# Kernel optimization log

Hardware: AMD Instinct MI355X
Metric: run time of the kernel (lower is better)

The kernel has to match this reference:

```python
import jax, jax.numpy as jnp
import numpy as np

B, H, W, C = 16, 96, 96, 128
FOCAL_LEVEL = 3
FOCAL_WINDOW = 3
FOCAL_FACTOR = 2
LN_EPS = 1e-3  # keras LayerNormalization default epsilon


def dwconv_same(x, k):
    # x: [B,H,W,C], k: [kh,kw,1,C] depthwise kernel (feature_group_count=C)
    return jax.lax.conv_general_dilated(
        x, k, window_strides=(1, 1), padding='SAME',
        dimension_numbers=('NHWC', 'HWIO', 'NHWC'),
        feature_group_count=x.shape[-1])


def setup_inputs() -> dict:
    key = jax.random.key(0)
    ks = jax.random.split(key, 12)
    s = 0.02
    out_f = 2 * C + (FOCAL_LEVEL + 1)
    inp = {
        'x': jax.random.normal(ks[0], (B, H, W, C), dtype=jnp.float32),
        'Wf': jax.random.normal(ks[1], (C, out_f), dtype=jnp.float32) * s,
        'bf': jnp.zeros((out_f,), dtype=jnp.float32),
        'Wh': jax.random.normal(ks[2], (C, C), dtype=jnp.float32) * s,
        'bh': jnp.zeros((C,), dtype=jnp.float32),
        'gamma': jnp.ones((C,), dtype=jnp.float32),
        'beta': jnp.zeros((C,), dtype=jnp.float32),
        'Wp': jax.random.normal(ks[3], (C, C), dtype=jnp.float32) * s,
        'bp': jnp.zeros((C,), dtype=jnp.float32),
    }
    for l in range(FOCAL_LEVEL):
        kk = FOCAL_FACTOR * l + FOCAL_WINDOW  # 3, 5, 7
        inp[f'k{l}'] = jax.random.normal(ks[4 + l], (kk, kk, 1, C), dtype=jnp.float32) * s
    return inp


def reference(x, Wf, bf, k0, k1, k2, Wh, bh, gamma, beta, Wp, bp):
    gelu = lambda t: jax.nn.gelu(t, approximate=False)  # keras gelu is exact
    y = jnp.einsum('bhwc,cd->bhwd', x, Wf) + bf  # f(): [B,H,W,2C+L+1]
    q = y[..., :C]
    ctx = y[..., C:2 * C]
    gates = y[..., 2 * C:]  # [B,H,W,L+1]

    ctx_all = jnp.zeros_like(ctx)
    for l, k in enumerate((k0, k1, k2)):
        ctx = gelu(dwconv_same(ctx, k))
        ctx_all = ctx_all + ctx * gates[..., l:l + 1]

    ctx_global = gelu(jnp.mean(ctx, axis=(1, 2), keepdims=True))  # [B,1,1,C]
    ctx_all = ctx_all + ctx_global * gates[..., FOCAL_LEVEL:]

    modulator = jnp.einsum('bhwc,cd->bhwd', ctx_all, Wh) + bh  # 1x1 conv h()
    x_out = q * modulator

    # post-LN over channel dim
    mu = jnp.mean(x_out, axis=-1, keepdims=True)
    var = jnp.mean(jnp.square(x_out - mu), axis=-1, keepdims=True)
    x_out = (x_out - mu) * jax.lax.rsqrt(var + LN_EPS) * gamma + beta

    x_out = jnp.einsum('bhwc,cd->bhwd', x_out, Wp) + bp  # proj (dropout p=0)
    return x_out
```

## Files before the change

### kernel.cpp

```cpp
#include <hip/hip_runtime.h>
#include <math.h>

#define B_ 16
#define H_ 96
#define W_ 96
#define C_ 128
#define HW_ (H_*W_)
#define NTOK (B_*HW_)
#define NOUT 260

#define TH 16
#define TW 32
#define B0H 28
#define B0W 44
#define B1H 26
#define B1W 42
#define B2H 22
#define B2W 38

typedef unsigned short ushort_t;
typedef unsigned int uint_t;
typedef float f32x4 __attribute__((ext_vector_type(4)));
typedef float f32x2 __attribute__((ext_vector_type(2)));
typedef short bfrag __attribute__((ext_vector_type(8)));
typedef unsigned short us8 __attribute__((ext_vector_type(8)));

__device__ __forceinline__ float gelu_f(float t) {
    return 0.5f * t * (1.0f + erff(t * 0.7071067811865475f));
}
__device__ __forceinline__ float b2f(ushort_t u) {
    union { unsigned int i; float f; } t; t.i = (unsigned int)u << 16; return t.f;
}
__device__ __forceinline__ ushort_t f2b(float f) {
    union { float f; unsigned int i; } t; t.f = f;
    unsigned int lsb = (t.i >> 16) & 1u;
    t.i += 0x7fffu + lsb;
    return (ushort_t)(t.i >> 16);
}
__device__ __forceinline__ uint_t pk2(float a, float b) {
    uint_t r;
    asm("v_cvt_pk_bf16_f32 %0, %1, %2" : "=v"(r) : "v"(a), "v"(b));
    return r;
}
__device__ __forceinline__ void unp2(uint_t u, float& a, float& b) {
    union { unsigned int i; float f; } x, y;
    x.i = u << 16; y.i = u & 0xffff0000u;
    a = x.f; b = y.f;
}
__device__ __forceinline__ void unp8(const uint4 v, float* f) {
    unp2(v.x, f[0], f[1]); unp2(v.y, f[2], f[3]);
    unp2(v.z, f[4], f[5]); unp2(v.w, f[6], f[7]);
}
__device__ __forceinline__ uint4 pk8(const float* f) {
    uint4 v;
    v.x = pk2(f[0], f[1]); v.y = pk2(f[2], f[3]);
    v.z = pk2(f[4], f[5]); v.w = pk2(f[6], f[7]);
    return v;
}
__device__ __forceinline__ f32x2 unp2p(uint_t u) {
    union { uint_t i; float f; } a, b;
    a.i = u << 16; b.i = u & 0xffff0000u;
    f32x2 r; r.x = a.f; r.y = b.f; return r;
}
__device__ __forceinline__ void unp8p(const uint4 v, f32x2* d) {
    d[0] = unp2p(v.x); d[1] = unp2p(v.y); d[2] = unp2p(v.z); d[3] = unp2p(v.w);
}

__device__ __forceinline__ void split8_to(const float* f,
                                          ushort_t* __restrict__ hdst,
                                          ushort_t* __restrict__ ldst) {
    uint_t hp[4], lp[4];
    #pragma unroll
    for (int j = 0; j < 4; ++j) {
        const float a = f[2*j], b = f[2*j+1];
        const uint_t h = pk2(a, b);
        union { uint_t i; float f; } ha, hb;
        ha.i = h << 16; hb.i = h & 0xffff0000u;
        hp[j] = h;
        lp[j] = pk2(a - ha.f, b - hb.f);
    }
    *(uint4*)hdst = make_uint4(hp[0], hp[1], hp[2], hp[3]);
    *(uint4*)ldst = make_uint4(lp[0], lp[1], lp[2], lp[3]);
}

__global__ __launch_bounds__(128) void pack_weights(
    const float* __restrict__ Wf, const float* __restrict__ Wh,
    const float* __restrict__ Wp, ushort_t* __restrict__ pk)
{
    const int n = blockIdx.x, mat = blockIdx.y, k = threadIdx.x;
    if (mat == 4 && n >= 16) return;
    float v;
    if (mat == 0)      v = Wf[(size_t)k * NOUT + n];
    else if (mat == 1) v = Wf[(size_t)k * NOUT + C_ + n];
    else if (mat == 2) v = Wh[(size_t)k * C_ + n];
    else if (mat == 3) v = Wp[(size_t)k * C_ + n];
    else               v = (n < 4) ? Wf[(size_t)k * NOUT + 2*C_ + n] : 0.0f;
    const ushort_t h = f2b(v);
    const ushort_t l = f2b(v - b2f(h));
    ushort_t* base = pk + (size_t)mat * (2 * C_ * C_);
    const int lo_off = (mat == 4) ? 16 * C_ : C_ * C_;
    base[n * C_ + k] = h;
    base[lo_off + n * C_ + k] = l;
}

template <bool A_LO>
__device__ __forceinline__ void mfma_gemm64(
    const ushort_t (*Ah)[136], const ushort_t (*Al)[136],
    const ushort_t* __restrict__ Bh, const ushort_t* __restrict__ Bl,
    int lane, int n0, f32x4 acc[4][2])
{
    const int ar = lane & 15;
    const int ak = (lane >> 4) << 3;
    #pragma unroll
    for (int kk = 0; kk < 4; ++kk) {
        const int kb = (kk << 5) + ak;
        const bfrag bh0 = *(const bfrag*)(Bh + (((n0      + ar) << 7) + kb));
        const bfrag bh1 = *(const bfrag*)(Bh + (((n0 + 16 + ar) << 7) + kb));
        const bfrag bl0 = *(const bfrag*)(Bl + (((n0      + ar) << 7) + kb));
        const bfrag bl1 = *(const bfrag*)(Bl + (((n0 + 16 + ar) << 7) + kb));
        #pragma unroll
        for (int m = 0; m < 4; ++m) {
            const bfrag ah = *(const bfrag*)&Ah[(m << 4) + ar][kb];
            if constexpr (A_LO) {
                const bfrag al = *(const bfrag*)&Al[(m << 4) + ar][kb];
                acc[m][0] = __builtin_amdgcn_mfma_f32_16x16x32_bf16(al, bh0, acc[m][0], 0, 0, 0);
                acc[m][1] = __builtin_amdgcn_mfma_f32_16x16x32_bf16(al, bh1, acc[m][1], 0, 0, 0);
            }
            acc[m][0] = __builtin_amdgcn_mfma_f32_16x16x32_bf16(ah, bl0, acc[m][0], 0, 0, 0);
            acc[m][1] = __builtin_amdgcn_mfma_f32_16x16x32_bf16(ah, bl1, acc[m][1], 0, 0, 0);
            acc[m][0] = __builtin_amdgcn_mfma_f32_16x16x32_bf16(ah, bh0, acc[m][0], 0, 0, 0);
            acc[m][1] = __builtin_amdgcn_mfma_f32_16x16x32_bf16(ah, bh1, acc[m][1], 0, 0, 0);
        }
    }
}

__device__ __forceinline__ void stage_split_f32(
    const float* __restrict__ src, int tid,
    ushort_t (*Ah)[136], ushort_t (*Al)[136])
{
    #pragma unroll
    for (int p = 0; p < 4; ++p) {
        const int i  = tid + (p << 8);
        const int t  = i >> 4;
        const int c8 = (i & 15) << 3;
        const float4 v0 = *(const float4*)(src + (size_t)t * C_ + c8);
        const float4 v1 = *(const float4*)(src + (size_t)t * C_ + c8 + 4);
        const float f[8] = {v0.x, v0.y, v0.z, v0.w, v1.x, v1.y, v1.z, v1.w};
        split8_to(f, &Ah[t][c8], &Al[t][c8]);
    }
}

__global__ __launch_bounds__(256) void gemm_ctx_gates_mfma(
    const float* __restrict__ x, const float* __restrict__ bf,
    const ushort_t* __restrict__ pk,
    ushort_t* __restrict__ ctx, float* __restrict__ gates,
    float* __restrict__ csum)
{
    __shared__ ushort_t Abuf[2][64][136];
    const int tid  = threadIdx.x;
    const int tok0 = blockIdx.x * 64;
    const int lane = tid & 63;
    const int n0   = (tid >> 6) << 5;

    if (blockIdx.x < 8) csum[blockIdx.x * 256 + tid] = 0.0f;

    stage_split_f32(x + (size_t)tok0 * C_, tid, Abuf[0], Abuf[1]);
    __syncthreads();

    f32x4 acc[4][2] = {};
    {
        const ushort_t* Bh = pk + (size_t)1 * (2 * C_ * C_);
        const ushort_t* Bl = Bh + C_ * C_;
        mfma_gemm64<true>(Abuf[0], Abuf[1], Bh, Bl, lane, n0, acc);
    }

    {
        const int w  = tid >> 6;
        const int ar = lane & 15;
        const int ak = (lane >> 4) << 3;
        const ushort_t* Gh = pk + (size_t)4 * (2 * C_ * C_);
        const ushort_t* Gl = Gh + 16 * C_;
        f32x4 gacc = {};
        #pragma unroll
        for (int kk = 0; kk < 4; ++kk) {
            const int kb = (kk << 5) + ak;
            const bfrag gh = *(const bfrag*)(Gh + ((ar << 7) + kb));
            const bfrag gl = *(const bfrag*)(Gl + ((ar << 7) + kb));
            const bfrag ah = *(const bfrag*)&Abuf[0][(w << 4) + ar][kb];
            const bfrag al = *(const bfrag*)&Abuf[1][(w << 4) + ar][kb];
            gacc = __builtin_amdgcn_mfma_f32_16x16x32_bf16(al, gh, gacc, 0, 0, 0);
            gacc = __builtin_amdgcn_mfma_f32_16x16x32_bf16(ah, gl, gacc, 0, 0, 0);
            gacc = __builtin_amdgcn_mfma_f32_16x16x32_bf16(ah, gh, gacc, 0, 0, 0);
        }
        if (ar < 4) {
            const int rg = (lane >> 4) << 2;
            #pragma unroll
            for (int r = 0; r < 4; ++r)
                gates[(size_t)(tok0 + (w << 4) + rg + r) * 4 + ar] = gacc[r] + bf[2*C_ + ar];
        }
    }
    __syncthreads();

    {
        const int ar = lane & 15;
        const int rg = (lane >> 4) << 2;
        #pragma unroll
        for (int n = 0; n < 2; ++n) {
            const int col = n0 + (n << 4) + ar;
            const float bias = bf[C_ + col];
            #pragma unroll
            for (int m = 0; m < 4; ++m) {
                const int rowb = (m << 4) + rg;
                const uint_t p0 = pk2(acc[m][n][0] + bias, acc[m][n][1] + bias);
                const uint_t p1 = pk2(acc[m][n][2] + bias, acc[m][n][3] + bias);
                Abuf[0][rowb + 0][col] = (ushort_t)p0;
                Abuf[0][rowb + 1][col] = (ushort_t)(p0 >> 16);
                Abuf[0][rowb + 2][col] = (ushort_t)p1;
                Abuf[0][rowb + 3][col] = (ushort_t)(p1 >> 16);
            }
        }
    }
    __syncthreads();

    #pragma unroll
    for (int p = 0; p < 4; ++p) {
        const int i  = tid + (p << 8);
        const int cg = i >> 6;
        const int t  = i & 63;
        *(uint4*)(ctx + (((size_t)cg * NTOK + tok0 + t) << 3))
            = *(const uint4*)&Abuf[0][t][cg << 3];
    }
}

__global__ __launch_bounds__(256, 4) void focal_conv_fused(
    const ushort_t* __restrict__ ctx_in,
    const float* __restrict__ k0w, const float* __restrict__ k1w,
    const float* __restrict__ k2w,
    const float* __restrict__ gates,
    ushort_t* __restrict__ ctx_all,
    float* __restrict__ csum)
{
    __shared__ uint4 bufA[B0H*B0W];
    __shared__ uint4 buf1[B1H*B1W];
    __shared__ float wts[(9+25+49)*8];

    const int tid  = threadIdx.x;
    const int cg   = blockIdx.x;
    const int tile = blockIdx.y;
    const int bb   = blockIdx.z;
    const int wt   = tile % 3, ht = tile / 3;
    const int c0   = cg << 3;
    const int h0   = ht * TH, w0 = wt * TW;

    if (tid < 166) {
        const int f = tid << 2;
        const float* src; int r;
        if (f < 72)       { r = f;       src = k0w; }
        else if (f < 272) { r = f - 72;  src = k1w; }
        else              { r = f - 272; src = k2w; }
        const int tap = r >> 3, off = r & 7;
        *(float4*)&wts[f] = *(const float4*)(src + tap * C_ + c0 + off);
    }

    const ushort_t* cin = ctx_in + (((size_t)cg * NTOK + (size_t)bb * HW_) << 3);
    for (int i = tid; i < B0H*B0W; i += 256) {
        const int r = i / B0W, q = i - r * B0W;
        const int hh = h0 - 6 + r, ww = w0 - 6 + q;
        uint4 v = make_uint4(0u, 0u, 0u, 0u);
        if ((unsigned)hh < (unsigned)H_ && (unsigned)ww < (unsigned)W_)
            v = *(const uint4*)(cin + ((size_t)(hh * W_ + ww) << 3));
        bufA[i] = v;
    }
    __syncthreads();

    {
        int iv[5], ecp[5], boff[5];
        #pragma unroll
        for (int p = 0; p < 5; ++p) {
            const int e = tid + (p << 8);
            iv[p] = (e < B1H*B1W);
            const int ec = iv[p] ? e : 0;
            ecp[p] = ec;
            boff[p] = (ec / B1W) * B0W + (ec % B1W);
        }
        f32x2 acc[5][4] = {};
        #pragma unroll 1
        for (int a = 0; a < 3; ++a) {
            #pragma unroll
            for (int b = 0; b < 3; ++b) {
                f32x2 wv[4];
                #pragma unroll
                for (int c = 0; c < 4; ++c)
                    wv[c] = *(const f32x2*)&wts[(a*3+b)*8 + 2*c];
                const int off = a * B0W + b;
                #pragma unroll
                for (int p = 0; p < 5; ++p) {
                    f32x2 d[4]; unp8p(bufA[boff[p] + off], d);
                    #pragma unroll
                    for (int c = 0; c < 4; ++c)
                        acc[p][c] = __builtin_elementwise_fma(d[c], wv[c], acc[p][c]);
                }
            }
        }
        __syncthreads();
        #pragma unroll
        for (int p = 0; p < 5; ++p) if (iv[p]) {
            float g[8];
            #pragma unroll
            for (int c = 0; c < 4; ++c) {
                g[2*c]   = gelu_f(acc[p][c].x);
                g[2*c+1] = gelu_f(acc[p][c].y);
            }
            buf1[ecp[p]] = pk8(g);
        }
    }
    __syncthreads();

    {
        int iv[4], ecp[4], boff[4];
        #pragma unroll
        for (int p = 0; p < 4; ++p) {
            const int e = tid + (p << 8);
            iv[p] = (e < B2H*B2W);
            const int ec = iv[p] ? e : 0;
            ecp[p] = ec;
            boff[p] = (ec / B2W) * B1W + (ec % B2W);
        }
        f32x2 acc[4][4] = {};
        #pragma unroll 1
        for (int a = 0; a < 5; ++a) {
            #pragma unroll
            for (int b = 0; b < 5; ++b) {
                f32x2 wv[4];
                #pragma unroll
                for (int c = 0; c < 4; ++c)
                    wv[c] = *(const f32x2*)&wts[72 + (a*5+b)*8 + 2*c];
                const int off = a * B1W + b;
                #pragma unroll
                for (int p = 0; p < 4; ++p) {
                    f32x2 d[4]; unp8p(buf1[boff[p] + off], d);
                    #pragma unroll
                    for (int c = 0; c < 4; ++c)
                        acc[p][c] = __builtin_elementwise_fma(d[c], wv[c], acc[p][c]);
                }
            }
        }
        __syncthreads();
        #pragma unroll
        for (int p = 0; p < 4; ++p) if (iv[p]) {
            float g[8];
            #pragma unroll
            for (int c = 0; c < 4; ++c) {
                g[2*c]   = gelu_f(acc[p][c].x);
                g[2*c+1] = gelu_f(acc[p][c].y);
            }
            bufA[ecp[p]] = pk8(g);
        }
    }
    __syncthreads();

    float lsum[8] = {};
    {
        const int th0 = tid >> 5, tw0 = tid & 31;
        f32x2 acc[2][4] = {};
        #pragma unroll 1
        for (int a = 0; a < 7; ++a) {
            #pragma unroll
            for (int b = 0; b < 7; ++b) {
                f32x2 wv[4];
                #pragma unroll
                for (int c = 0; c < 4; ++c)
                    wv[c] = *(const f32x2*)&wts[272 + (a*7+b)*8 + 2*c];
                #pragma unroll
                for (int p = 0; p < 2; ++p) {
                    const int th = th0 + (p << 3);
                    f32x2 d[4]; unp8p(bufA[(th + a)*B2W + (tw0 + b)], d);
                    #pragma unroll
                    for (int c = 0; c < 4; ++c)
                        acc[p][c] = __builtin_elementwise_fma(d[c], wv[c], acc[p][c]);
                }
            }
        }
        #pragma unroll
        for (int p = 0; p < 2; ++p) {
            const int th = th0 + (p << 3);
            float ctx3[8];
            #pragma unroll
            for (int c = 0; c < 4; ++c) {
                ctx3[2*c]   = gelu_f(acc[p][c].x);
                ctx3[2*c+1] = gelu_f(acc[p][c].y);
            }
            #pragma unroll
            for (int c = 0; c < 8; ++c) lsum[c] += ctx3[c];
            float d1[8]; unp8(buf1[(5+th)*B1W + (5+tw0)], d1);
            float d2[8]; unp8(bufA[(th+3)*B2W + (tw0+3)], d2);
            const size_t pix = (size_t)bb * HW_ + (size_t)(h0 + th) * W_ + (w0 + tw0);
            const float4 gt = *(const float4*)(gates + pix * 4);
            float o[8];
            #pragma unroll
            for (int c = 0; c < 8; ++c)
                o[c] = d1[c] * gt.x + d2[c] * gt.y + ctx3[c] * gt.z;
            *(uint4*)(ctx_all + pix * C_ + c0) = pk8(o);
        }
    }

    __syncthreads();
    float* red = (float*)bufA;
    #pragma unroll
    for (int c = 0; c < 8; ++c) red[c*256 + tid] = lsum[c];
    __syncthreads();
    for (int off = 128; off > 0; off >>= 1) {
        if (tid < off) {
            #pragma unroll
            for (int c = 0; c < 8; ++c)
                red[c*256 + tid] += red[c*256 + tid + off];
        }
        __syncthreads();
    }
    if (tid < 8) atomicAdd(&csum[bb * C_ + c0 + tid], red[tid * 256]);
}

__global__ __launch_bounds__(128) void glob_mod(
    const float* __restrict__ csum, const float* __restrict__ Wh,
    float* __restrict__ whc)
{
    __shared__ float cg[128];
    const int b = blockIdx.x, n = threadIdx.x;
    cg[n] = gelu_f(csum[b * C_ + n] * (1.0f / (float)HW_));
    __syncthreads();
    float s = 0.f;
    #pragma unroll 8
    for (int k = 0; k < C_; ++k)
        s = fmaf(cg[k], Wh[(size_t)k * C_ + n], s);
    whc[b * C_ + n] = s;
}

__global__ __launch_bounds__(256) void modq_ln_out_mfma(
    const ushort_t* __restrict__ ctx_all, const float* __restrict__ whc,
    const float* __restrict__ gates, const float* __restrict__ x,
    const ushort_t* __restrict__ pk, const float* __restrict__ bf,
    const float* __restrict__ bh, const float* __restrict__ gamma,
    const float* __restrict__ beta, const float* __restrict__ bp,
    float* __restrict__ out)
{
    __shared__ ushort_t Abuf[2][64][136];
    __shared__ float g3s[64];
    __shared__ float whcs[128];
    __shared__ float mu_s[64];
    __shared__ float rs_s[64];
    __shared__ f32x2 part[64][4];
    float (*xs)[132] = (float(*)[132])&Abuf[0][0][0];
    ushort_t (*xlnb)[136] = (ushort_t(*)[136])&Abuf[0][0][0];

    const int tid  = threadIdx.x;
    const int tok0 = blockIdx.x * 64;
    const int bidx = tok0 / HW_;
    const int lane = tid & 63;
    const int n0   = (tid >> 6) << 5;
    const int ar   = lane & 15;
    const int rg   = (lane >> 4) << 2;

    #pragma unroll
    for (int p = 0; p < 4; ++p) {
        const int i  = tid + (p << 8);
        const int t  = i >> 4;
        const int c8 = (i & 15) << 3;
        *(us8*)&Abuf[0][t][c8] = *(const us8*)(ctx_all + (size_t)(tok0 + t) * C_ + c8);
    }
    if (tid < 64)           g3s[tid]        = gates[(size_t)(tok0 + tid) * 4 + 3];
    else if (tid < 192)     whcs[tid - 64]  = whc[bidx * C_ + (tid - 64)];
    __syncthreads();

    f32x4 am[4][2] = {};
    {
        const ushort_t* Bh2 = pk + (size_t)2 * (2 * C_ * C_);
        const ushort_t* Bl2 = Bh2 + C_ * C_;
        mfma_gemm64<false>(Abuf[0], Abuf[0], Bh2, Bl2, lane, n0, am);
    }
    __syncthreads();

    stage_split_f32(x + (size_t)tok0 * C_, tid, Abuf[0], Abuf[1]);
    __syncthreads();

    f32x4 aq[4][2] = {};
    {
        const ushort_t* Bh0 = pk;
        const ushort_t* Bl0 = Bh0 + C_ * C_;
        mfma_gemm64<true>(Abuf[0], Abuf[1], Bh0, Bl0, lane, n0, aq);
    }
    __syncthreads();

    {
        #pragma unroll
        for (int n = 0; n < 2; ++n) {
            const int col = n0 + (n << 4) + ar;
            const float bfv = bf[col];
            const float bhv = bh[col];
            const float whv = whcs[col];
            #pragma unroll
            for (int m = 0; m < 4; ++m)
                #pragma unroll
                for (int r = 0; r < 4; ++r) {
                    const int row = (m << 4) + rg + r;
                    const float mod = am[m][n][r] + g3s[row] * whv + bhv;
                    xs[row][col] = (aq[m][n][r] + bfv) * mod;
                }
        }
    }
    __syncthreads();

    {
        const int tt = tid >> 2;
        const int qq = tid & 3;
        float s = 0.f, s2 = 0.f;
        #pragma unroll
        for (int c = 0; c < 32; c += 4) {
            const float4 v = *(const float4*)&xs[tt][(qq << 5) + c];
            s  += v.x + v.y + v.z + v.w;
            s2 += v.x*v.x + v.y*v.y + v.z*v.z + v.w*v.w;
        }
        f32x2 pr; pr.x = s; pr.y = s2;
        part[tt][qq] = pr;
    }
    __syncthreads();
    if (tid < 64) {
        const f32x2 p0 = part[tid][0], p1 = part[tid][1];
        const f32x2 p2 = part[tid][2], p3 = part[tid][3];
        const float s  = (p0.x + p1.x) + (p2.x + p3.x);
        const float s2 = (p0.y + p1.y) + (p2.y + p3.y);
        const float mu  = s * (1.0f / 128.0f);
        const float var = s2 * (1.0f / 128.0f) - mu * mu;
        mu_s[tid] = mu;
        rs_s[tid] = rsqrtf(var + 0.001f);
    }
    __syncthreads();

    {
        const int tt = tid >> 2;
        const int c0b = (tid & 3) << 5;
        const float mu = mu_s[tt], rs = rs_s[tt];
        uint_t xw[16];
        #pragma unroll
        for (int j = 0; j < 8; ++j) {
            const int c = c0b + (j << 2);
            const float4 v  = *(const float4*)&xs[tt][c];
            const float4 gm = *(const float4*)(gamma + c);
            const float4 bt = *(const float4*)(beta + c);
            xw[2*j]   = pk2((v.x - mu) * rs * gm.x + bt.x,
                            (v.y - mu) * rs * gm.y + bt.y);
            xw[2*j+1] = pk2((v.z - mu) * rs * gm.z + bt.z,
                            (v.w - mu) * rs * gm.w + bt.w);
        }
        __syncthreads();
        #pragma unroll
        for (int j = 0; j < 4; ++j)
            *(uint4*)&xlnb[tt][c0b + (j << 3)] = *(uint4*)&xw[4*j];
    }
    __syncthreads();

    f32x4 ao[4][2] = {};
    {
        const ushort_t* Bh3 = pk + (size_t)3 * (2 * C_ * C_);
        const ushort_t* Bl3 = Bh3 + C_ * C_;
        mfma_gemm64<false>((const ushort_t(*)[136])xlnb,
                           (const ushort_t(*)[136])xlnb, Bh3, Bl3, lane, n0, ao);
    }
    {
        #pragma unroll
        for (int n = 0; n < 2; ++n) {
            const int col = n0 + (n << 4) + ar;
            const float bpv = bp[col];
            #pragma unroll
            for (int m = 0; m < 4; ++m)
                #pragma unroll
                for (int r = 0; r < 4; ++r) {
                    const int row = (m << 4) + rg + r;
                    out[(size_t)(tok0 + row) * C_ + col] = ao[m][n][r] + bpv;
                }
        }
    }
}

extern "C" void kernel_launch(void* const* d_in, const int* in_sizes, int n_in,
                              void* d_out, int out_size, void* d_ws, size_t ws_size,
                              hipStream_t stream) {
    const float* x     = (const float*)d_in[0];
    const float* Wf    = (const float*)d_in[1];
    const float* bf    = (const float*)d_in[2];
    const float* Wh    = (const float*)d_in[3];
    const float* bh    = (const float*)d_in[4];
    const float* gamma = (const float*)d_in[5];
    const float* beta  = (const float*)d_in[6];
    const float* Wp    = (const float*)d_in[7];
    const float* bp    = (const float*)d_in[8];
    const float* k0    = (const float*)d_in[9];
    const float* k1    = (const float*)d_in[10];
    const float* k2    = (const float*)d_in[11];
    float* out = (float*)d_out;

    const size_t NC = (size_t)NTOK * C_;
    ushort_t* P0  = (ushort_t*)d_ws;
    ushort_t* ACC = P0 + NC;
    float* gates  = (float*)(ACC + NC);
    float* csum   = gates + (size_t)NTOK * 4;
    float* whc    = csum + (size_t)B_ * C_;
    ushort_t* pkw = (ushort_t*)(whc + (size_t)B_ * C_);

    pack_weights<<<dim3(C_, 5), 128, 0, stream>>>(Wf, Wh, Wp, pkw);
    gemm_ctx_gates_mfma<<<NTOK / 64, 256, 0, stream>>>(x, bf, pkw, P0, gates, csum);
    focal_conv_fused<<<dim3(C_/8, (H_/TH)*(W_/TW), B_), 256, 0, stream>>>(
        P0, k0, k1, k2, gates, ACC, csum);
    glob_mod<<<B_, 128, 0, stream>>>(csum, Wh, whc);
    modq_ln_out_mfma<<<NTOK / 64, 256, 0, stream>>>(
        ACC, whc, gates, x, pkw, bf, bh, gamma, beta, bp, out);
}
```

Before: 405.7 us.

## Switch intermediates and MFMA operands from bf16 to fp16 with mixed-precision FMAs

Replaces bf16 storage and MFMA with fp16 across all GEMMs, intermediate buffers and the depthwise-conv stages. The depthwise conv inner loops now use v_fma_mix_f32 to multiply packed fp16 data by packed fp16 weights directly into fp32 accumulators, which removes the explicit unpacking instructions and halves the shared-memory weight footprint. The cost is fp16 range limits: values above about 65504 overflow, and the pkrtz conversion truncates toward zero instead of rounding to nearest.

```diff
diff --git a/kernel.cpp b/kernel.cpp
--- a/kernel.cpp
+++ b/kernel.cpp
@@ -22,48 +22,44 @@
 typedef unsigned int uint_t;
 typedef float f32x4 __attribute__((ext_vector_type(4)));
 typedef float f32x2 __attribute__((ext_vector_type(2)));
-typedef short bfrag __attribute__((ext_vector_type(8)));
+typedef __fp16 fp16x2 __attribute__((ext_vector_type(2)));
+typedef _Float16 h16x8 __attribute__((ext_vector_type(8)));
 typedef unsigned short us8 __attribute__((ext_vector_type(8)));
 
 __device__ __forceinline__ float gelu_f(float t) {
     return 0.5f * t * (1.0f + erff(t * 0.7071067811865475f));
 }
-__device__ __forceinline__ float b2f(ushort_t u) {
-    union { unsigned int i; float f; } t; t.i = (unsigned int)u << 16; return t.f;
-}
-__device__ __forceinline__ ushort_t f2b(float f) {
-    union { float f; unsigned int i; } t; t.f = f;
-    unsigned int lsb = (t.i >> 16) & 1u;
-    t.i += 0x7fffu + lsb;
-    return (ushort_t)(t.i >> 16);
-}
-__device__ __forceinline__ uint_t pk2(float a, float b) {
-    uint_t r;
-    asm("v_cvt_pk_bf16_f32 %0, %1, %2" : "=v"(r) : "v"(a), "v"(b));
-    return r;
-}
-__device__ __forceinline__ void unp2(uint_t u, float& a, float& b) {
-    union { unsigned int i; float f; } x, y;
-    x.i = u << 16; y.i = u & 0xffff0000u;
-    a = x.f; b = y.f;
-}
-__device__ __forceinline__ void unp8(const uint4 v, float* f) {
-    unp2(v.x, f[0], f[1]); unp2(v.y, f[2], f[3]);
-    unp2(v.z, f[4], f[5]); unp2(v.w, f[6], f[7]);
-}
-__device__ __forceinline__ uint4 pk8(const float* f) {
+
+__device__ __forceinline__ uint_t pkh2(float a, float b) {
+    union { fp16x2 h; uint_t u; } c;
+    c.h = __builtin_amdgcn_cvt_pkrtz(a, b);
+    return c.u;
+}
+__device__ __forceinline__ uint4 pkh8(const float* f) {
     uint4 v;
-    v.x = pk2(f[0], f[1]); v.y = pk2(f[2], f[3]);
-    v.z = pk2(f[4], f[5]); v.w = pk2(f[6], f[7]);
+    v.x = pkh2(f[0], f[1]); v.y = pkh2(f[2], f[3]);
+    v.z = pkh2(f[4], f[5]); v.w = pkh2(f[6], f[7]);
     return v;
 }
-__device__ __forceinline__ f32x2 unp2p(uint_t u) {
-    union { uint_t i; float f; } a, b;
-    a.i = u << 16; b.i = u & 0xffff0000u;
-    f32x2 r; r.x = a.f; r.y = b.f; return r;
-}
-__device__ __forceinline__ void unp8p(const uint4 v, f32x2* d) {
-    d[0] = unp2p(v.x); d[1] = unp2p(v.y); d[2] = unp2p(v.z); d[3] = unp2p(v.w);
+__device__ __forceinline__ void unph2(uint_t u, float& a, float& b) {
+    union { uint_t u; _Float16 h[2]; } c; c.u = u;
+    a = (float)c.h[0]; b = (float)c.h[1];
+}
+__device__ __forceinline__ void unph8(const uint4 v, float* f) {
+    unph2(v.x, f[0], f[1]); unph2(v.y, f[2], f[3]);
+    unph2(v.z, f[4], f[5]); unph2(v.w, f[6], f[7]);
+}
+
+__device__ __forceinline__ void fmix2(float& a0, float& a1, uint_t d, uint_t w) {
+    asm("v_fma_mix_f32 %0, %2, %3, %0 op_sel_hi:[1,1,0]\n\t"
+        "v_fma_mix_f32 %1, %2, %3, %1 op_sel:[1,1,0] op_sel_hi:[1,1,0]"
+        : "+v"(a0), "+v"(a1) : "v"(d), "v"(w));
+}
+__device__ __forceinline__ void fmix8(float* acc, const uint4 d, const uint4 w) {
+    fmix2(acc[0], acc[1], d.x, w.x);
+    fmix2(acc[2], acc[3], d.y, w.y);
+    fmix2(acc[4], acc[5], d.z, w.z);
+    fmix2(acc[6], acc[7], d.w, w.w);
 }
 
 __device__ __forceinline__ void split8_to(const float* f,
@@ -73,11 +69,10 @@
     #pragma unroll
     for (int j = 0; j < 4; ++j) {
         const float a = f[2*j], b = f[2*j+1];
-        const uint_t h = pk2(a, b);
-        union { uint_t i; float f; } ha, hb;
-        ha.i = h << 16; hb.i = h & 0xffff0000u;
+        const uint_t h = pkh2(a, b);
+        float ha, hb; unph2(h, ha, hb);
         hp[j] = h;
-        lp[j] = pk2(a - ha.f, b - hb.f);
+        lp[j] = pkh2(a - ha, b - hb);
     }
     *(uint4*)hdst = make_uint4(hp[0], hp[1], hp[2], hp[3]);
     *(uint4*)ldst = make_uint4(lp[0], lp[1], lp[2], lp[3]);
@@ -95,12 +90,13 @@
     else if (mat == 2) v = Wh[(size_t)k * C_ + n];
     else if (mat == 3) v = Wp[(size_t)k * C_ + n];
     else               v = (n < 4) ? Wf[(size_t)k * NOUT + 2*C_ + n] : 0.0f;
-    const ushort_t h = f2b(v);
-    const ushort_t l = f2b(v - b2f(h));
+    union { _Float16 h; ushort_t s; } ch, cl;
+    ch.h = (_Float16)v;
+    cl.h = (_Float16)(v - (float)ch.h);
     ushort_t* base = pk + (size_t)mat * (2 * C_ * C_);
     const int lo_off = (mat == 4) ? 16 * C_ : C_ * C_;
-    base[n * C_ + k] = h;
-    base[lo_off + n * C_ + k] = l;
+    base[n * C_ + k] = ch.s;
+    base[lo_off + n * C_ + k] = cl.s;
 }
 
 template <bool A_LO>
@@ -114,22 +110,22 @@
     #pragma unroll
     for (int kk = 0; kk < 4; ++kk) {
         const int kb = (kk << 5) + ak;
-        const bfrag bh0 = *(const bfrag*)(Bh + (((n0      + ar) << 7) + kb));
-        const bfrag bh1 = *(const bfrag*)(Bh + (((n0 + 16 + ar) << 7) + kb));
-        const bfrag bl0 = *(const bfrag*)(Bl + (((n0      + ar) << 7) + kb));
-        const bfrag bl1 = *(const bfrag*)(Bl + (((n0 + 16 + ar) << 7) + kb));
+        const h16x8 bh0 = *(const h16x8*)(Bh + (((n0      + ar) << 7) + kb));
+        const h16x8 bh1 = *(const h16x8*)(Bh + (((n0 + 16 + ar) << 7) + kb));
+        const h16x8 bl0 = *(const h16x8*)(Bl + (((n0      + ar) << 7) + kb));
+        const h16x8 bl1 = *(const h16x8*)(Bl + (((n0 + 16 + ar) << 7) + kb));
         #pragma unroll
         for (int m = 0; m < 4; ++m) {
-            const bfrag ah = *(const bfrag*)&Ah[(m << 4) + ar][kb];
+            const h16x8 ah = *(const h16x8*)&Ah[(m << 4) + ar][kb];
             if constexpr (A_LO) {
-                const bfrag al = *(const bfrag*)&Al[(m << 4) + ar][kb];
-                acc[m][0] = __builtin_amdgcn_mfma_f32_16x16x32_bf16(al, bh0, acc[m][0], 0, 0, 0);
-                acc[m][1] = __builtin_amdgcn_mfma_f32_16x16x32_bf16(al, bh1, acc[m][1], 0, 0, 0);
+                const h16x8 al = *(const h16x8*)&Al[(m << 4) + ar][kb];
+                acc[m][0] = __builtin_amdgcn_mfma_f32_16x16x32_f16(al, bh0, acc[m][0], 0, 0, 0);
+                acc[m][1] = __builtin_amdgcn_mfma_f32_16x16x32_f16(al, bh1, acc[m][1], 0, 0, 0);
             }
-            acc[m][0] = __builtin_amdgcn_mfma_f32_16x16x32_bf16(ah, bl0, acc[m][0], 0, 0, 0);
-            acc[m][1] = __builtin_amdgcn_mfma_f32_16x16x32_bf16(ah, bl1, acc[m][1], 0, 0, 0);
-            acc[m][0] = __builtin_amdgcn_mfma_f32_16x16x32_bf16(ah, bh0, acc[m][0], 0, 0, 0);
-            acc[m][1] = __builtin_amdgcn_mfma_f32_16x16x32_bf16(ah, bh1, acc[m][1], 0, 0, 0);
+            acc[m][0] = __builtin_amdgcn_mfma_f32_16x16x32_f16(ah, bl0, acc[m][0], 0, 0, 0);
+            acc[m][1] = __builtin_amdgcn_mfma_f32_16x16x32_f16(ah, bl1, acc[m][1], 0, 0, 0);
+            acc[m][0] = __builtin_amdgcn_mfma_f32_16x16x32_f16(ah, bh0, acc[m][0], 0, 0, 0);
+            acc[m][1] = __builtin_amdgcn_mfma_f32_16x16x32_f16(ah, bh1, acc[m][1], 0, 0, 0);
         }
     }
 }
@@ -184,13 +180,13 @@
         #pragma unroll
         for (int kk = 0; kk < 4; ++kk) {
             const int kb = (kk << 5) + ak;
-            const bfrag gh = *(const bfrag*)(Gh + ((ar << 7) + kb));
-            const bfrag gl = *(const bfrag*)(Gl + ((ar << 7) + kb));
-            const bfrag ah = *(const bfrag*)&Abuf[0][(w << 4) + ar][kb];
-            const bfrag al = *(const bfrag*)&Abuf[1][(w << 4) + ar][kb];
-            gacc = __builtin_amdgcn_mfma_f32_16x16x32_bf16(al, gh, gacc, 0, 0, 0);
-            gacc = __builtin_amdgcn_mfma_f32_16x16x32_bf16(ah, gl, gacc, 0, 0, 0);
-            gacc = __builtin_amdgcn_mfma_f32_16x16x32_bf16(ah, gh, gacc, 0, 0, 0);
+            const h16x8 gh = *(const h16x8*)(Gh + ((ar << 7) + kb));
+            const h16x8 gl = *(const h16x8*)(Gl + ((ar << 7) + kb));
+            const h16x8 ah = *(const h16x8*)&Abuf[0][(w << 4) + ar][kb];
+            const h16x8 al = *(const h16x8*)&Abuf[1][(w << 4) + ar][kb];
+            gacc = __builtin_amdgcn_mfma_f32_16x16x32_f16(al, gh, gacc, 0, 0, 0);
+            gacc = __builtin_amdgcn_mfma_f32_16x16x32_f16(ah, gl, gacc, 0, 0, 0);
+            gacc = __builtin_amdgcn_mfma_f32_16x16x32_f16(ah, gh, gacc, 0, 0, 0);
         }
         if (ar < 4) {
             const int rg = (lane >> 4) << 2;
@@ -211,8 +207,8 @@
             #pragma unroll
             for (int m = 0; m < 4; ++m) {
                 const int rowb = (m << 4) + rg;
-                const uint_t p0 = pk2(acc[m][n][0] + bias, acc[m][n][1] + bias);
-                const uint_t p1 = pk2(acc[m][n][2] + bias, acc[m][n][3] + bias);
+                const uint_t p0 = pkh2(acc[m][n][0] + bias, acc[m][n][1] + bias);
+                const uint_t p1 = pkh2(acc[m][n][2] + bias, acc[m][n][3] + bias);
                 Abuf[0][rowb + 0][col] = (ushort_t)p0;
                 Abuf[0][rowb + 1][col] = (ushort_t)(p0 >> 16);
                 Abuf[0][rowb + 2][col] = (ushort_t)p1;
@@ -242,7 +238,7 @@
 {
     __shared__ uint4 bufA[B0H*B0W];
     __shared__ uint4 buf1[B1H*B1W];
-    __shared__ float wts[(9+25+49)*8];
+    __shared__ uint_t wtsu[(9+25+49)*4];
 
     const int tid  = threadIdx.x;
     const int cg   = blockIdx.x;
@@ -259,7 +255,8 @@
         else if (f < 272) { r = f - 72;  src = k1w; }
         else              { r = f - 272; src = k2w; }
         const int tap = r >> 3, off = r & 7;
-        *(float4*)&wts[f] = *(const float4*)(src + tap * C_ + c0 + off);
+        const float4 v = *(const float4*)(src + tap * C_ + c0 + off);
+        *(uint2*)&wtsu[f >> 1] = make_uint2(pkh2(v.x, v.y), pkh2(v.z, v.w));
     }
 
     const ushort_t* cin = ctx_in + (((size_t)cg * NTOK + (size_t)bb * HW_) << 3);
@@ -283,23 +280,16 @@
             ecp[p] = ec;
             boff[p] = (ec / B1W) * B0W + (ec % B1W);
         }
-        f32x2 acc[5][4] = {};
+        float acc[5][8] = {};
         #pragma unroll 1
         for (int a = 0; a < 3; ++a) {
             #pragma unroll
             for (int b = 0; b < 3; ++b) {
-                f32x2 wv[4];
-                #pragma unroll
-                for (int c = 0; c < 4; ++c)
-                    wv[c] = *(const f32x2*)&wts[(a*3+b)*8 + 2*c];
+                const uint4 wq = *(const uint4*)&wtsu[(a*3+b) << 2];
                 const int off = a * B0W + b;
                 #pragma unroll
-                for (int p = 0; p < 5; ++p) {
-                    f32x2 d[4]; unp8p(bufA[boff[p] + off], d);
-                    #pragma unroll
-                    for (int c = 0; c < 4; ++c)
-                        acc[p][c] = __builtin_elementwise_fma(d[c], wv[c], acc[p][c]);
-                }
+                for (int p = 0; p < 5; ++p)
+                    fmix8(acc[p], bufA[boff[p] + off], wq);
             }
         }
         __syncthreads();
@@ -307,11 +297,8 @@
         for (int p = 0; p < 5; ++p) if (iv[p]) {
             float g[8];
             #pragma unroll
-            for (int c = 0; c < 4; ++c) {
-                g[2*c]   = gelu_f(acc[p][c].x);
-                g[2*c+1] = gelu_f(acc[p][c].y);
-            }
-            buf1[ecp[p]] = pk8(g);
+            for (int c = 0; c < 8; ++c) g[c] = gelu_f(acc[p][c]);
+            buf1[ecp[p]] = pkh8(g);
         }
     }
     __syncthreads();
@@ -326,23 +313,16 @@
             ecp[p] = ec;
             boff[p] = (ec / B2W) * B1W + (ec % B2W);
         }
-        f32x2 acc[4][4] = {};
+        float acc[4][8] = {};
         #pragma unroll 1
         for (int a = 0; a < 5; ++a) {
             #pragma unroll
             for (int b = 0; b < 5; ++b) {
-                f32x2 wv[4];
-                #pragma unroll
-                for (int c = 0; c < 4; ++c)
-                    wv[c] = *(const f32x2*)&wts[72 + (a*5+b)*8 + 2*c];
+                const uint4 wq = *(const uint4*)&wtsu[36 + ((a*5+b) << 2)];
                 const int off = a * B1W + b;
                 #pragma unroll
-                for (int p = 0; p < 4; ++p) {
-                    f32x2 d[4]; unp8p(buf1[boff[p] + off], d);
-                    #pragma unroll
-                    for (int c = 0; c < 4; ++c)
-                        acc[p][c] = __builtin_elementwise_fma(d[c], wv[c], acc[p][c]);
-                }
+                for (int p = 0; p < 4; ++p)
+                    fmix8(acc[p], buf1[boff[p] + off], wq);
             }
         }
         __syncthreads();
@@ -350,11 +330,8 @@
         for (int p = 0; p < 4; ++p) if (iv[p]) {
             float g[8];
             #pragma unroll
-            for (int c = 0; c < 4; ++c) {
-                g[2*c]   = gelu_f(acc[p][c].x);
-                g[2*c+1] = gelu_f(acc[p][c].y);
-            }
-            bufA[ecp[p]] = pk8(g);
+            for (int c = 0; c < 8; ++c) g[c] = gelu_f(acc[p][c]);
+            bufA[ecp[p]] = pkh8(g);
         }
     }
     __syncthreads();
@@ -362,22 +339,16 @@
     float lsum[8] = {};
     {
         const int th0 = tid >> 5, tw0 = tid & 31;
-        f32x2 acc[2][4] = {};
+        float acc[2][8] = {};
         #pragma unroll 1
         for (int a = 0; a < 7; ++a) {
             #pragma unroll
             for (int b = 0; b < 7; ++b) {
-                f32x2 wv[4];
-                #pragma unroll
-                for (int c = 0; c < 4; ++c)
-                    wv[c] = *(const f32x2*)&wts[272 + (a*7+b)*8 + 2*c];
+                const uint4 wq = *(const uint4*)&wtsu[136 + ((a*7+b) << 2)];
                 #pragma unroll
                 for (int p = 0; p < 2; ++p) {
                     const int th = th0 + (p << 3);
-                    f32x2 d[4]; unp8p(bufA[(th + a)*B2W + (tw0 + b)], d);
-                    #pragma unroll
-                    for (int c = 0; c < 4; ++c)
-                        acc[p][c] = __builtin_elementwise_fma(d[c], wv[c], acc[p][c]);
+                    fmix8(acc[p], bufA[(th + a)*B2W + (tw0 + b)], wq);
                 }
             }
         }
@@ -386,21 +357,16 @@
             const int th = th0 + (p << 3);
             float ctx3[8];
             #pragma unroll
-            for (int c = 0; c < 4; ++c) {
-                ctx3[2*c]   = gelu_f(acc[p][c].x);
-                ctx3[2*c+1] = gelu_f(acc[p][c].y);
-            }
-            #pragma unroll
-            for (int c = 0; c < 8; ++c) lsum[c] += ctx3[c];
-            float d1[8]; unp8(buf1[(5+th)*B1W + (5+tw0)], d1);
-            float d2[8]; unp8(bufA[(th+3)*B2W + (tw0+3)], d2);
+            for (int c = 0; c < 8; ++c) { ctx3[c] = gelu_f(acc[p][c]); lsum[c] += ctx3[c]; }
+            float d1[8]; unph8(buf1[(5+th)*B1W + (5+tw0)], d1);
+            float d2[8]; unph8(bufA[(th+3)*B2W + (tw0+3)], d2);
             const size_t pix = (size_t)bb * HW_ + (size_t)(h0 + th) * W_ + (w0 + tw0);
             const float4 gt = *(const float4*)(gates + pix * 4);
             float o[8];
             #pragma unroll
             for (int c = 0; c < 8; ++c)
                 o[c] = d1[c] * gt.x + d2[c] * gt.y + ctx3[c] * gt.z;
-            *(uint4*)(ctx_all + pix * C_ + c0) = pk8(o);
+            *(uint4*)(ctx_all + pix * C_ + c0) = pkh8(o);
         }
     }
 
@@ -546,10 +512,10 @@
             const float4 v  = *(const float4*)&xs[tt][c];
             const float4 gm = *(const float4*)(gamma + c);
             const float4 bt = *(const float4*)(beta + c);
-            xw[2*j]   = pk2((v.x - mu) * rs * gm.x + bt.x,
-                            (v.y - mu) * rs * gm.y + bt.y);
-            xw[2*j+1] = pk2((v.z - mu) * rs * gm.z + bt.z,
-                            (v.w - mu) * rs * gm.w + bt.w);
+            xw[2*j]   = pkh2((v.x - mu) * rs * gm.x + bt.x,
+                             (v.y - mu) * rs * gm.y + bt.y);
+            xw[2*j+1] = pkh2((v.z - mu) * rs * gm.z + bt.z,
+                             (v.w - mu) * rs * gm.w + bt.w);
         }
         __syncthreads();
         #pragma unroll
```

Measured after the change: 381.9 us. -5.9%, faster.
